# Optimization experiments

Hardware: AMD Instinct MI355X
Metric: run time of the kernel (lower is better)

Reference implementation:

```python
import jax, jax.numpy as jnp
import numpy as np

N = 100000
CTX = 128
TGT = 32
H = 64
FUS = H + H // 2  # 96
E1 = 1600000
E2 = 800000
LN_EPS = 1e-5


def _gelu(x):
    return jax.nn.gelu(x, approximate=False)  # torch default is exact erf GELU


def _layer_norm(x, g, b):
    mu = jnp.mean(x, -1, keepdims=True)
    xc = x - mu
    var = jnp.mean(xc * xc, -1, keepdims=True)
    return xc * jax.lax.rsqrt(var + LN_EPS) * g + b


def _gcn_conv(x, W, b, ei, n):
    # PyG GCNConv: x' = D^-1/2 (A + I) D^-1/2 (x W) + b, with unit edge weights.
    h = x @ W  # [N, out]
    src, dst = ei[0], ei[1]
    deg = jnp.zeros((n,), h.dtype).at[dst].add(1.0) + 1.0  # +1 for self-loop
    dinv = jax.lax.rsqrt(deg)
    norm = dinv[src] * dinv[dst]  # [E]
    agg = jnp.zeros_like(h).at[dst].add(h[src] * norm[:, None])
    agg = agg + h * (dinv * dinv)[:, None]  # self-loop messages
    return agg + b


def setup_inputs() -> dict:
    key = jax.random.key(0)
    ks = jax.random.split(key, 32)
    def lin(k, fan_in, fan_out):
        s = 1.0 / np.sqrt(fan_in)
        k1, k2 = jax.random.split(k)
        return (jax.random.uniform(k1, (fan_in, fan_out), jnp.float32, -s, s),
                jax.random.uniform(k2, (fan_out,), jnp.float32, -s, s))
    inp = {}
    inp['context'] = jax.random.normal(ks[0], (N, CTX), jnp.float32)
    inp['target'] = jax.random.normal(ks[1], (N, TGT), jnp.float32)
    inp['mask'] = jax.random.bernoulli(ks[2], 0.5, (N, TGT))
    inp['adj_ei'] = jax.random.randint(ks[3], (2, E1), 0, N, jnp.int64 if jax.config.jax_enable_x64 else jnp.int32)
    inp['transit_ei'] = jax.random.randint(ks[4], (2, E2), 0, N, jnp.int64 if jax.config.jax_enable_x64 else jnp.int32)
    inp['mask_token'] = jax.random.normal(ks[5], (1, TGT), jnp.float32) * 0.01
    inp['ce_W1'], inp['ce_b1'] = lin(ks[6], CTX, H)
    inp['ce_g'] = jnp.ones((H,), jnp.float32)
    inp['ce_beta'] = jnp.zeros((H,), jnp.float32)
    inp['ce_W2'], inp['ce_b2'] = lin(ks[7], H, H)
    inp['te_W'], inp['te_b'] = lin(ks[8], TGT, H // 2)
    inp['g1_W'], inp['g1_b'] = lin(ks[9], FUS, H)
    inp['g2_W'], inp['g2_b'] = lin(ks[10], H, H)
    inp['t1_W'], inp['t1_b'] = lin(ks[11], FUS, H)
    inp['t2_W'], inp['t2_b'] = lin(ks[12], H, H)
    inp['alpha'] = jnp.float32(0.5)
    inp['h_W1'], inp['h_b1'] = lin(ks[13], H + FUS, H)
    inp['h_g'] = jnp.ones((H,), jnp.float32)
    inp['h_beta'] = jnp.zeros((H,), jnp.float32)
    inp['h_W2'], inp['h_b2'] = lin(ks[14], H, TGT)
    return inp


def reference(context, target, mask, adj_ei, transit_ei, mask_token,
              ce_W1, ce_b1, ce_g, ce_beta, ce_W2, ce_b2,
              te_W, te_b,
              g1_W, g1_b, g2_W, g2_b,
              t1_W, t1_b, t2_W, t2_b,
              alpha,
              h_W1, h_b1, h_g, h_beta, h_W2, h_b2):
    n = context.shape[0]
    # context encoder (eval mode: dropout is identity)
    c = _gelu(_layer_norm(context @ ce_W1 + ce_b1, ce_g, ce_beta))
    ctx = _gelu(c @ ce_W2 + ce_b2)
    # masked target encoder
    m = mask.astype(target.dtype)
    masked_t = target * (1.0 - m) + mask_token * m
    tgt = _gelu(masked_t @ te_W + te_b)
    fused = jnp.concatenate([ctx, tgt], -1)  # [N, 96]
    # spatial branch
    h1 = _gelu(_gcn_conv(fused, g1_W, g1_b, adj_ei, n))
    h_sp = _gcn_conv(h1, g2_W, g2_b, adj_ei, n)
    # transit branch
    h2 = _gelu(_gcn_conv(fused, t1_W, t1_b, transit_ei, n))
    h_tr = _gcn_conv(h2, t2_W, t2_b, transit_ei, n)
    a = jax.nn.sigmoid(alpha)
    h = a * h_sp + (1.0 - a) * h_tr
    z = jnp.concatenate([h, fused], -1)  # [N, 160]
    z = _gelu(_layer_norm(z @ h_W1 + h_b1, h_g, h_beta))
    return z @ h_W2 + h_b2  # [N, 32]
```

## Files before the change

kernel.cpp:

```cpp
#include <hip/hip_runtime.h>
#include <math.h>


#define LN_EPS 1e-5f
#define NRANGES 512
#define RMASK 511
#define LSHIFT 9
#define PASSP_EDGES 8192
#define GSTRIDE 16

typedef __attribute__((ext_vector_type(8))) short short8;
typedef __attribute__((ext_vector_type(4))) float float4v;
typedef __attribute__((ext_vector_type(4))) unsigned short ushort4v;

__device__ __forceinline__ float gelu_exact(float x) {
    return 0.5f * x * (1.0f + erff(x * 0.70710678118654752440f));
}

__device__ __forceinline__ float qsum16(float v) {
#pragma unroll
    for (int m = 1; m < 16; m <<= 1)
        v += __shfl_xor(v, m, 64);
    return v;
}

__device__ __forceinline__ int load_edge(const void* ei, int is32, long idx) {
    return is32 ? ((const int*)ei)[idx] : (int)((const long long*)ei)[idx];
}

__device__ __forceinline__ unsigned short f32_to_bf16(float f) {
    unsigned int x = __float_as_uint(f);
    x += 0x7fffu + ((x >> 16) & 1u);
    return (unsigned short)(x >> 16);
}
__device__ __forceinline__ float bf16_to_f32(unsigned short u) {
    return __uint_as_float((unsigned int)u << 16);
}

__device__ __forceinline__ void load_dst4(const void* ei1, int e1, const void* ei2, int e2,
                                          int n, int is32, int base, int nv, int nd[4]) {
    if (is32 && nv == 4) {
        if (base + 3 < e1 && (((e1 + base) & 3) == 0)) {
            int4 v = *(const int4*)((const int*)ei1 + (size_t)e1 + base);
            nd[0] = v.x; nd[1] = v.y; nd[2] = v.z; nd[3] = v.w;
            return;
        }
        if (base >= e1 && (((e2 + base - e1) & 3) == 0)) {
            int4 v = *(const int4*)((const int*)ei2 + (size_t)e2 + (base - e1));
            nd[0] = v.x + n; nd[1] = v.y + n; nd[2] = v.z + n; nd[3] = v.w + n;
            return;
        }
    }
#pragma unroll
    for (int u = 0; u < 4; ++u) {
        int i = base + u;
        if (u >= nv) { nd[u] = -1; continue; }
        if (i < e1) nd[u] = load_edge(ei1, is32, (long)e1 + i);
        else        nd[u] = load_edge(ei2, is32, (long)e2 + (i - e1)) + n;
    }
}

__device__ __forceinline__ void load_src4(const void* ei1, int e1, const void* ei2, int e2,
                                          int is32, int base, int nv, int ns[4]) {
    if (is32 && nv == 4) {
        if (base + 3 < e1 && ((base & 3) == 0)) {
            int4 v = *(const int4*)((const int*)ei1 + base);
            ns[0] = v.x; ns[1] = v.y; ns[2] = v.z; ns[3] = v.w;
            return;
        }
        if (base >= e1 && (((base - e1) & 3) == 0)) {
            int4 v = *(const int4*)((const int*)ei2 + (base - e1));
            ns[0] = v.x; ns[1] = v.y; ns[2] = v.z; ns[3] = v.w;
            return;
        }
    }
#pragma unroll
    for (int u = 0; u < 4; ++u) {
        int i = base + u;
        if (u >= nv) { ns[u] = 0; continue; }
        if (i < e1) ns[u] = load_edge(ei1, is32, i);
        else        ns[u] = load_edge(ei2, is32, (long)(i - e1));
    }
}

__global__ __launch_bounds__(256) void detect_kernel(const unsigned char* __restrict__ mask_bytes,
                                                     const int* __restrict__ ei_words,
                                                     int* __restrict__ flags,
                                                     int* __restrict__ gcur, int cap) {
    if (blockIdx.x == 0) {
        __shared__ int f0, f1;
        if (threadIdx.x == 0) { f0 = 0; f1 = 0; }
        __syncthreads();
        int i = threadIdx.x;
        if ((i & 3) != 0 && mask_bytes[i] != 0) f0 = 1;
        if (i < 64 && ei_words[2 * i + 1] != 0) f1 = 1;
        __syncthreads();
        if (threadIdx.x == 0) { flags[0] = f0; flags[1] = f1; }
    } else {
        int r = (blockIdx.x - 1) * 256 + threadIdx.x;
        if (r < NRANGES) gcur[r * GSTRIDE] = r * cap;
    }
}

__device__ __forceinline__ void passp_body(
    const void* ei1, int e1, const void* ei2, int e2,
    int n, const int* flags, int* gcur, int cap, unsigned* ebuf, int sbits, int bid)
{
    __shared__ int hist[NRANGES];
    __shared__ int base[NRANGES];
    const int E = e1 + e2;
    const int is32 = flags[1];
    const int b0 = bid * PASSP_EDGES;
    const int bend = (b0 + PASSP_EDGES < E) ? b0 + PASSP_EDGES : E;

    for (int k = threadIdx.x; k < NRANGES; k += 256) hist[k] = 0;
    __syncthreads();

    int nd[32], rk[32];
#pragma unroll
    for (int j = 0; j < 8; ++j) {
        int bi = b0 + j * 1024 + (int)threadIdx.x * 4;
        int nv = bend - bi; nv = (nv < 0) ? 0 : (nv > 4 ? 4 : nv);
        load_dst4(ei1, e1, ei2, e2, n, is32, bi, nv, &nd[j * 4]);
#pragma unroll
        for (int u = 0; u < 4; ++u)
            if (u < nv) rk[j * 4 + u] = atomicAdd(&hist[nd[j * 4 + u] & RMASK], 1);
    }
    __syncthreads();

    for (int r = threadIdx.x; r < NRANGES; r += 256) {
        int c = hist[r];
        base[r] = c ? atomicAdd(&gcur[r * GSTRIDE], c) : 0;
    }
    __syncthreads();

#pragma unroll
    for (int j = 0; j < 8; ++j) {
        int bi = b0 + j * 1024 + (int)threadIdx.x * 4;
        int nv = bend - bi; nv = (nv < 0) ? 0 : (nv > 4 ? 4 : nv);
        int sv[4];
        load_src4(ei1, e1, ei2, e2, is32, bi, nv, sv);
#pragma unroll
        for (int u = 0; u < 4; ++u) {
            if (u < nv) {
                int d = nd[j * 4 + u];
                int r = d & RMASK;
                int pos = base[r] + rk[j * 4 + u];
                if (pos < (r + 1) * cap)
                    ebuf[pos] = (unsigned)sv[u] | ((unsigned)(d >> LSHIFT) << sbits);
            }
        }
    }
}

__device__ __forceinline__ void prep_body(
    const float* context, const float* target, const void* mask, const int* flags,
    const float* mask_token, const float* te_W, const float* te_b,
    unsigned short* ctxb, unsigned short* fused, int n, int bid)
{
    __shared__ float tbuf[32][32];
    int w = threadIdx.x >> 6;
    int j = threadIdx.x & 63;
    int r0 = __builtin_amdgcn_readfirstlane(bid * 32 + w * 8);
    if (r0 >= n) return;

    const float4* src = (const float4*)(context + (size_t)r0 * 128);
    ushort4v* dst = (ushort4v*)(ctxb + (size_t)r0 * 128);
#pragma unroll
    for (int p = 0; p < 4; ++p) {
        float4 v = src[p * 64 + j];
        ushort4v o;
        o.x = f32_to_bf16(v.x); o.y = f32_to_bf16(v.y);
        o.z = f32_to_bf16(v.z); o.w = f32_to_bf16(v.w);
        dst[p * 64 + j] = o;
    }

    int tr = j >> 5;
    int tj = j & 31;
#pragma unroll
    for (int rr = 0; rr < 4; ++rr) {
        int r = tr + rr * 2;
        long mi = (long)(r0 + r) * 32 + tj;
        int mraw = flags[0] ? (int)((const unsigned char*)mask)[mi]
                            : ((const int*)mask)[mi];
        float m = mraw ? 1.0f : 0.0f;
        tbuf[w * 8 + r][tj] = target[mi] * (1.0f - m) + mask_token[tj] * m;
    }

#pragma unroll
    for (int rr = 0; rr < 4; ++rr) {
        int r = tr + rr * 2;
        float y3 = te_b[tj];
#pragma unroll
        for (int k = 0; k < 32; ++k)
            y3 = fmaf(tbuf[w * 8 + r][k], te_W[k * 32 + tj], y3);
        fused[(long)(r0 + r) * 96 + 64 + tj] = f32_to_bf16(gelu_exact(y3));
    }
}

__global__ __launch_bounds__(256) void passp_prep_kernel(
    const void* __restrict__ ei1, int e1, const void* __restrict__ ei2, int e2,
    int n, const int* __restrict__ flags, int* __restrict__ gcur, int cap,
    unsigned* __restrict__ ebuf, int sbits, int ppBlocks,
    const float* __restrict__ context, const float* __restrict__ target,
    const void* __restrict__ mask, const float* __restrict__ mask_token,
    const float* __restrict__ te_W, const float* __restrict__ te_b,
    unsigned short* __restrict__ ctxb, unsigned short* __restrict__ fused)
{
    if ((int)blockIdx.x < ppBlocks)
        passp_body(ei1, e1, ei2, e2, n, flags, gcur, cap, ebuf, sbits, blockIdx.x);
    else
        prep_body(context, target, mask, flags, mask_token, te_W, te_b,
                  ctxb, fused, n, blockIdx.x - ppBlocks);
}

__device__ __forceinline__ void rscan_body(const int* gcur, int cap,
                                           int* rstart, int* rowptr, int n2) {
    __shared__ int ws[256];
    int t = threadIdx.x;
    int i0 = 2 * t, i1 = 2 * t + 1;
    int a0 = gcur[i0 * GSTRIDE] - i0 * cap;
    int a1 = gcur[i1 * GSTRIDE] - i1 * cap;
    ws[t] = a0 + a1;
    __syncthreads();
    for (int off = 1; off < 256; off <<= 1) {
        int v = (t >= off) ? ws[t - off] : 0;
        __syncthreads();
        if (t >= off) ws[t] += v;
        __syncthreads();
    }
    int ex = t ? ws[t - 1] : 0;
    rstart[i0] = ex;
    rstart[i1] = ex + a0;
    if (t == 255) { rstart[NRANGES] = ws[255]; rowptr[n2] = ws[255]; }
}

__device__ __forceinline__ void mfma_ln_body(
    const unsigned short* x, const float* W, const float* bias, const float* g,
    const float* beta, unsigned short* y, int n, int bid, int nblk)
{
    constexpr int K = 128, KS = K / 32, STRIDE = K + 8;
    __shared__ __align__(16) unsigned short wt[64 * STRIDE];
    int n0 = threadIdx.x & 63;
    int kk = threadIdx.x >> 6;
    for (int k = kk; k < K; k += 4)
        wt[n0 * STRIDE + k] = f32_to_bf16(W[k * 64 + n0]);
    __syncthreads();

    int w = threadIdx.x >> 6;
    int lane = threadIdx.x & 63;
    int c = lane & 15;
    int q = lane >> 4;

    short8 bfrag[KS][4];
#pragma unroll
    for (int s = 0; s < KS; ++s)
#pragma unroll
        for (int nt = 0; nt < 4; ++nt)
            bfrag[s][nt] = *(const short8*)&wt[(nt * 16 + c) * STRIDE + s * 32 + q * 8];

    float bs[4], gs[4], be[4];
#pragma unroll
    for (int nt = 0; nt < 4; ++nt) {
        bs[nt] = bias[nt * 16 + c];
        gs[nt] = g[nt * 16 + c];
        be[nt] = beta[nt * 16 + c];
    }

    int T = n >> 4;
    int stride = nblk * 4;
    for (int t = __builtin_amdgcn_readfirstlane(bid * 4 + w); t < T; t += stride) {
        int r0 = t << 4;
        const unsigned short* xa = x + (size_t)(r0 + c) * K + q * 8;
        float4v acc[4] = {{0,0,0,0},{0,0,0,0},{0,0,0,0},{0,0,0,0}};
#pragma unroll
        for (int s = 0; s < KS; ++s) {
            short8 a = *(const short8*)(xa + s * 32);
#pragma unroll
            for (int nt = 0; nt < 4; ++nt)
                acc[nt] = __builtin_amdgcn_mfma_f32_16x16x32_bf16(a, bfrag[s][nt], acc[nt], 0, 0, 0);
        }
#pragma unroll
        for (int reg = 0; reg < 4; ++reg) {
            float v0 = acc[0][reg] + bs[0];
            float v1 = acc[1][reg] + bs[1];
            float v2 = acc[2][reg] + bs[2];
            float v3 = acc[3][reg] + bs[3];
            float mean = qsum16((v0 + v1) + (v2 + v3)) * (1.0f / 64.0f);
            float x0 = v0 - mean, x1 = v1 - mean, x2 = v2 - mean, x3 = v3 - mean;
            float var = qsum16((x0 * x0 + x1 * x1) + (x2 * x2 + x3 * x3)) * (1.0f / 64.0f);
            float rstd = rsqrtf(var + LN_EPS);
            size_t row = (size_t)(r0 + q * 4 + reg) * 64;
            y[row + 0 * 16 + c] = f32_to_bf16(gelu_exact(x0 * rstd * gs[0] + be[0]));
            y[row + 1 * 16 + c] = f32_to_bf16(gelu_exact(x1 * rstd * gs[1] + be[1]));
            y[row + 2 * 16 + c] = f32_to_bf16(gelu_exact(x2 * rstd * gs[2] + be[2]));
            y[row + 3 * 16 + c] = f32_to_bf16(gelu_exact(x3 * rstd * gs[3] + be[3]));
        }
    }
}

__global__ __launch_bounds__(256) void ln_rscan_kernel(
    const unsigned short* __restrict__ x, const float* __restrict__ W,
    const float* __restrict__ bias, const float* __restrict__ g,
    const float* __restrict__ beta, unsigned short* __restrict__ y, int n, int nblk,
    const int* __restrict__ gcur, int cap, int* __restrict__ rstart,
    int* __restrict__ rowptr, int n2)
{
    if ((int)blockIdx.x == nblk)
        rscan_body(gcur, cap, rstart, rowptr, n2);
    else
        mfma_ln_body(x, W, bias, g, beta, y, n, blockIdx.x, nblk);
}

__device__ __forceinline__ void passq_body(
    const int* rstart, const unsigned* ebuf, int cap, int n2, int sbits,
    int* rowptr, int* rowcnt, float* dinv, int* srcs, int g)
{
    __shared__ int deg[NRANGES];
    __shared__ int cur[NRANGES];
    __shared__ int ws[256];
    const int t = threadIdx.x;
    const int gbase = rstart[g];
    const int total = rstart[g + 1] - gbase;
    const unsigned* eb = ebuf + (size_t)g * cap;
    const unsigned smask = (1u << sbits) - 1u;

    deg[2 * t] = 0; deg[2 * t + 1] = 0;
    __syncthreads();
    for (int i = t; i < total; i += 256)
        atomicAdd(&deg[eb[i] >> sbits], 1);
    __syncthreads();

    int a0 = deg[2 * t], a1 = deg[2 * t + 1];
    ws[t] = a0 + a1;
    __syncthreads();
    for (int off = 1; off < 256; off <<= 1) {
        int v = (t >= off) ? ws[t - off] : 0;
        __syncthreads();
        if (t >= off) ws[t] += v;
        __syncthreads();
    }
    int ex = t ? ws[t - 1] : 0;
    cur[2 * t] = ex;
    cur[2 * t + 1] = ex + a0;
    int node0 = ((2 * t) << LSHIFT) | g;
    int node1 = ((2 * t + 1) << LSHIFT) | g;
    if (node0 < n2) { rowptr[node0] = gbase + ex;      rowcnt[node0] = a0; dinv[node0] = rsqrtf((float)a0 + 1.0f); }
    if (node1 < n2) { rowptr[node1] = gbase + ex + a0; rowcnt[node1] = a1; dinv[node1] = rsqrtf((float)a1 + 1.0f); }
    __syncthreads();

    for (int i = t; i < total; i += 256) {
        unsigned e = eb[i];
        int rk = atomicAdd(&cur[e >> sbits], 1);
        srcs[gbase + rk] = (int)(e & smask);
    }
}

__device__ __forceinline__ void mfma_gelu_body(
    const unsigned short* x, const float* W, const float* bias,
    unsigned short* y, int n, int bid, int nblk)
{
    constexpr int K = 64, KS = K / 32, STRIDE = K + 8;
    __shared__ __align__(16) unsigned short wt[64 * STRIDE];
    int n0 = threadIdx.x & 63;
    int kk = threadIdx.x >> 6;
    for (int k = kk; k < K; k += 4)
        wt[n0 * STRIDE + k] = f32_to_bf16(W[k * 64 + n0]);
    __syncthreads();

    int w = threadIdx.x >> 6;
    int lane = threadIdx.x & 63;
    int c = lane & 15;
    int q = lane >> 4;

    short8 bfrag[KS][4];
#pragma unroll
    for (int s = 0; s < KS; ++s)
#pragma unroll
        for (int nt = 0; nt < 4; ++nt)
            bfrag[s][nt] = *(const short8*)&wt[(nt * 16 + c) * STRIDE + s * 32 + q * 8];

    float bs[4];
#pragma unroll
    for (int nt = 0; nt < 4; ++nt) bs[nt] = bias[nt * 16 + c];

    int T = n >> 4;
    int stride = nblk * 4;
    for (int t = __builtin_amdgcn_readfirstlane(bid * 4 + w); t < T; t += stride) {
        int r0 = t << 4;
        const unsigned short* xa = x + (size_t)(r0 + c) * K + q * 8;
        float4v acc[4] = {{0,0,0,0},{0,0,0,0},{0,0,0,0},{0,0,0,0}};
#pragma unroll
        for (int s = 0; s < KS; ++s) {
            short8 a = *(const short8*)(xa + s * 32);
#pragma unroll
            for (int nt = 0; nt < 4; ++nt)
                acc[nt] = __builtin_amdgcn_mfma_f32_16x16x32_bf16(a, bfrag[s][nt], acc[nt], 0, 0, 0);
        }
#pragma unroll
        for (int nt = 0; nt < 4; ++nt)
#pragma unroll
            for (int reg = 0; reg < 4; ++reg)
                y[(size_t)(r0 + q * 4 + reg) * 96 + nt * 16 + c] =
                    f32_to_bf16(gelu_exact(acc[nt][reg] + bs[nt]));
    }
}

__global__ __launch_bounds__(256) void passq_gelu_kernel(
    const int* __restrict__ rstart, const unsigned* __restrict__ ebuf, int cap, int n2,
    int sbits, int* __restrict__ rowptr, int* __restrict__ rowcnt,
    float* __restrict__ dinv, int* __restrict__ srcs,
    const unsigned short* __restrict__ x, const float* __restrict__ W,
    const float* __restrict__ bias, unsigned short* __restrict__ y, int n, int nblk)
{
    if ((int)blockIdx.x < NRANGES)
        passq_body(rstart, ebuf, cap, n2, sbits, rowptr, rowcnt, dinv, srcs, blockIdx.x);
    else
        mfma_gelu_body(x, W, bias, y, n, blockIdx.x - NRANGES, nblk);
}

__global__ __launch_bounds__(256) void mm_l1_dual_kernel(
    const unsigned short* __restrict__ x, const float* __restrict__ Wg,
    const float* __restrict__ Wt, const float* __restrict__ dinv,
    unsigned short* __restrict__ yg, unsigned short* __restrict__ yt, int n)
{
    constexpr int K = 96, KS = K / 32, STRIDE = K + 8;
    __shared__ __align__(16) unsigned short wtg[64 * STRIDE];
    __shared__ __align__(16) unsigned short wtt[64 * STRIDE];
    int n0 = threadIdx.x & 63;
    int kk = threadIdx.x >> 6;
    for (int k = kk; k < K; k += 4) {
        wtg[n0 * STRIDE + k] = f32_to_bf16(Wg[k * 64 + n0]);
        wtt[n0 * STRIDE + k] = f32_to_bf16(Wt[k * 64 + n0]);
    }
    __syncthreads();

    int w = threadIdx.x >> 6;
    int lane = threadIdx.x & 63;
    int c = lane & 15;
    int q = lane >> 4;

    short8 bg[KS][4], bt[KS][4];
#pragma unroll
    for (int s = 0; s < KS; ++s)
#pragma unroll
        for (int nt = 0; nt < 4; ++nt) {
            bg[s][nt] = *(const short8*)&wtg[(nt * 16 + c) * STRIDE + s * 32 + q * 8];
            bt[s][nt] = *(const short8*)&wtt[(nt * 16 + c) * STRIDE + s * 32 + q * 8];
        }

    int T = n >> 4;
    int stride = gridDim.x * 4;
    for (int t = __builtin_amdgcn_readfirstlane(blockIdx.x * 4 + w); t < T; t += stride) {
        int r0 = t << 4;
        const unsigned short* xa = x + (size_t)(r0 + c) * K + q * 8;
        float4v ag[4] = {{0,0,0,0},{0,0,0,0},{0,0,0,0},{0,0,0,0}};
        float4v at[4] = {{0,0,0,0},{0,0,0,0},{0,0,0,0},{0,0,0,0}};
#pragma unroll
        for (int s = 0; s < KS; ++s) {
            short8 a = *(const short8*)(xa + s * 32);
#pragma unroll
            for (int nt = 0; nt < 4; ++nt) {
                ag[nt] = __builtin_amdgcn_mfma_f32_16x16x32_bf16(a, bg[s][nt], ag[nt], 0, 0, 0);
                at[nt] = __builtin_amdgcn_mfma_f32_16x16x32_bf16(a, bt[s][nt], at[nt], 0, 0, 0);
            }
        }
        float sg[4], st[4];
#pragma unroll
        for (int reg = 0; reg < 4; ++reg) {
            sg[reg] = dinv[r0 + q * 4 + reg];
            st[reg] = dinv[n + r0 + q * 4 + reg];
        }
#pragma unroll
        for (int nt = 0; nt < 4; ++nt)
#pragma unroll
            for (int reg = 0; reg < 4; ++reg) {
                size_t row = (size_t)(r0 + q * 4 + reg) * 64 + nt * 16 + c;
                yg[row] = f32_to_bf16(ag[nt][reg] * sg[reg]);
                yt[row] = f32_to_bf16(at[nt][reg] * st[reg]);
            }
    }
}

__device__ __forceinline__ void mm64_body(const unsigned short* x, const float* W,
                                          const float* scale, unsigned short* y,
                                          int n, int bid, int nblk) {
    constexpr int K = 64, KS = K / 32, STRIDE = K + 8;
    __shared__ __align__(16) unsigned short wt[64 * STRIDE];
    int n0 = threadIdx.x & 63;
    int kk = threadIdx.x >> 6;
    for (int k = kk; k < K; k += 4)
        wt[n0 * STRIDE + k] = f32_to_bf16(W[k * 64 + n0]);
    __syncthreads();

    int w = threadIdx.x >> 6;
    int lane = threadIdx.x & 63;
    int c = lane & 15;
    int q = lane >> 4;

    short8 bfrag[KS][4];
#pragma unroll
    for (int s = 0; s < KS; ++s)
#pragma unroll
        for (int nt = 0; nt < 4; ++nt)
            bfrag[s][nt] = *(const short8*)&wt[(nt * 16 + c) * STRIDE + s * 32 + q * 8];

    int T = n >> 4;
    int stride = nblk * 4;
    for (int t = __builtin_amdgcn_readfirstlane(bid * 4 + w); t < T; t += stride) {
        int r0 = t << 4;
        const unsigned short* xa = x + (size_t)(r0 + c) * K + q * 8;
        float4v acc[4] = {{0,0,0,0},{0,0,0,0},{0,0,0,0},{0,0,0,0}};
#pragma unroll
        for (int s = 0; s < KS; ++s) {
            short8 a = *(const short8*)(xa + s * 32);
#pragma unroll
            for (int nt = 0; nt < 4; ++nt)
                acc[nt] = __builtin_amdgcn_mfma_f32_16x16x32_bf16(a, bfrag[s][nt], acc[nt], 0, 0, 0);
        }
        float sc[4];
#pragma unroll
        for (int reg = 0; reg < 4; ++reg)
            sc[reg] = scale[r0 + q * 4 + reg];
#pragma unroll
        for (int nt = 0; nt < 4; ++nt)
#pragma unroll
            for (int reg = 0; reg < 4; ++reg)
                y[(size_t)(r0 + q * 4 + reg) * 64 + nt * 16 + c] = f32_to_bf16(acc[nt][reg] * sc[reg]);
    }
}

__global__ __launch_bounds__(256) void mm_l2_kernel(
    const unsigned short* __restrict__ xg, const unsigned short* __restrict__ xt,
    const float* __restrict__ Wg, const float* __restrict__ Wt,
    const float* __restrict__ dinv,
    unsigned short* __restrict__ yg, unsigned short* __restrict__ yt, int n, int nblk)
{
    if ((int)blockIdx.x < nblk)
        mm64_body(xg, Wg, dinv, yg, n, blockIdx.x, nblk);
    else
        mm64_body(xt, Wt, dinv + n, yt, n, blockIdx.x - nblk, nblk);
}

__device__ __forceinline__ float gather_row(const int* srcs, const unsigned short* lin,
                                            int beg, int cnt, int j) {
    float acc = 0.0f;
    for (int base = beg; base < beg + cnt; base += 64) {
        int c2 = beg + cnt - base;
        if (c2 > 64) c2 = 64;
        int sj = (j < c2) ? srcs[base + j] : 0;
        int t = 0;
        for (; t + 8 <= c2; t += 8) {
            float v[8];
#pragma unroll
            for (int u = 0; u < 8; ++u) {
                int s = __shfl(sj, t + u, 64);
                v[u] = bf16_to_f32(lin[(long)s * 64 + j]);
            }
            acc += ((v[0] + v[1]) + (v[2] + v[3])) + ((v[4] + v[5]) + (v[6] + v[7]));
        }
        for (; t < c2; ++t) {
            int s = __shfl(sj, t, 64);
            acc += bf16_to_f32(lin[(long)s * 64 + j]);
        }
    }
    return acc;
}

__global__ __launch_bounds__(256) void gather_l1_kernel(
    const int* __restrict__ rowptr, const int* __restrict__ rowcnt,
    const int* __restrict__ srcs, const float* __restrict__ dinv,
    const unsigned short* __restrict__ ling, const unsigned short* __restrict__ lint,
    const float* __restrict__ bg, const float* __restrict__ bt,
    unsigned short* __restrict__ h1g, unsigned short* __restrict__ h1t, int n)
{
    int w = threadIdx.x >> 6;
    int j = threadIdx.x & 63;
    int node = __builtin_amdgcn_readfirstlane(blockIdx.x * 4 + w);
    if (node >= n) return;
    long oi = (long)node * 64 + j;

    float ag = gather_row(srcs, ling, rowptr[node], rowcnt[node], j);
    float pg = fmaf(dinv[node], ag + bf16_to_f32(ling[oi]), bg[j]);
    h1g[oi] = f32_to_bf16(gelu_exact(pg));

    int tn = n + node;
    float at = gather_row(srcs, lint, rowptr[tn], rowcnt[tn], j);
    float pt = fmaf(dinv[tn], at + bf16_to_f32(lint[oi]), bt[j]);
    h1t[oi] = f32_to_bf16(gelu_exact(pt));
}

__global__ __launch_bounds__(256) void gather_l2_kernel(
    const int* __restrict__ rowptr, const int* __restrict__ rowcnt,
    const int* __restrict__ srcs, const float* __restrict__ dinv,
    const unsigned short* __restrict__ ling, const unsigned short* __restrict__ lint,
    const float* __restrict__ bg, const float* __restrict__ bt,
    const float* __restrict__ alpha_ptr, unsigned short* __restrict__ hb, int n)
{
    int w = threadIdx.x >> 6;
    int j = threadIdx.x & 63;
    int node = __builtin_amdgcn_readfirstlane(blockIdx.x * 4 + w);
    if (node >= n) return;
    long oi = (long)node * 64 + j;

    float ag = gather_row(srcs, ling, rowptr[node], rowcnt[node], j);
    float pg = fmaf(dinv[node], ag + bf16_to_f32(ling[oi]), bg[j]);

    int tn = n + node;
    float at = gather_row(srcs, lint, rowptr[tn], rowcnt[tn], j);
    float pt = fmaf(dinv[tn], at + bf16_to_f32(lint[oi]), bt[j]);

    float a = 1.0f / (1.0f + expf(-alpha_ptr[0]));
    hb[oi] = f32_to_bf16(a * pg + (1.0f - a) * pt);
}

__global__ __launch_bounds__(256) void head_mfma_kernel(
    const unsigned short* __restrict__ hb, const unsigned short* __restrict__ fused,
    const float* __restrict__ h_W1, const float* __restrict__ h_b1,
    const float* __restrict__ h_g, const float* __restrict__ h_beta,
    const float* __restrict__ h_W2, const float* __restrict__ h_b2,
    float* __restrict__ out, int n)
{
    constexpr int ST1 = 168;
    constexpr int ST2 = 72;
    __shared__ __align__(16) unsigned short wt1[64 * ST1];
    __shared__ __align__(16) unsigned short wt2[32 * ST2];
    __shared__ __align__(16) unsigned short zl[4][16 * ST2];

    int n0 = threadIdx.x & 63;
    int kk = threadIdx.x >> 6;
    for (int k = kk; k < 160; k += 4)
        wt1[n0 * ST1 + k] = f32_to_bf16(h_W1[k * 64 + n0]);
    if (n0 < 32)
        for (int k = kk; k < 64; k += 4)
            wt2[n0 * ST2 + k] = f32_to_bf16(h_W2[k * 32 + n0]);
    __syncthreads();

    int w = threadIdx.x >> 6;
    int lane = threadIdx.x & 63;
    int c = lane & 15;
    int q = lane >> 4;

    short8 b1f[5][4];
#pragma unroll
    for (int s = 0; s < 5; ++s)
#pragma unroll
        for (int nt = 0; nt < 4; ++nt)
            b1f[s][nt] = *(const short8*)&wt1[(nt * 16 + c) * ST1 + s * 32 + q * 8];
    short8 b2f[2][2];
#pragma unroll
    for (int s = 0; s < 2; ++s)
#pragma unroll
        for (int nt = 0; nt < 2; ++nt)
            b2f[s][nt] = *(const short8*)&wt2[(nt * 16 + c) * ST2 + s * 32 + q * 8];

    float bs[4], gs[4], be[4];
#pragma unroll
    for (int nt = 0; nt < 4; ++nt) {
        bs[nt] = h_b1[nt * 16 + c];
        gs[nt] = h_g[nt * 16 + c];
        be[nt] = h_beta[nt * 16 + c];
    }
    float b2s[2];
#pragma unroll
    for (int nt = 0; nt < 2; ++nt) b2s[nt] = h_b2[nt * 16 + c];

    unsigned short* zw = zl[w];
    int T = n >> 4;
    int stride = gridDim.x * 4;
    for (int t = __builtin_amdgcn_readfirstlane(blockIdx.x * 4 + w); t < T; t += stride) {
        int r0 = t << 4;
        const unsigned short* xh = hb + (size_t)(r0 + c) * 64 + q * 8;
        const unsigned short* xf = fused + (size_t)(r0 + c) * 96 + q * 8;
        float4v acc[4] = {{0,0,0,0},{0,0,0,0},{0,0,0,0},{0,0,0,0}};
#pragma unroll
        for (int s = 0; s < 2; ++s) {
            short8 a = *(const short8*)(xh + s * 32);
#pragma unroll
            for (int nt = 0; nt < 4; ++nt)
                acc[nt] = __builtin_amdgcn_mfma_f32_16x16x32_bf16(a, b1f[s][nt], acc[nt], 0, 0, 0);
        }
#pragma unroll
        for (int s = 0; s < 3; ++s) {
            short8 a = *(const short8*)(xf + s * 32);
#pragma unroll
            for (int nt = 0; nt < 4; ++nt)
                acc[nt] = __builtin_amdgcn_mfma_f32_16x16x32_bf16(a, b1f[2 + s][nt], acc[nt], 0, 0, 0);
        }
#pragma unroll
        for (int reg = 0; reg < 4; ++reg) {
            float v0 = acc[0][reg] + bs[0];
            float v1 = acc[1][reg] + bs[1];
            float v2 = acc[2][reg] + bs[2];
            float v3 = acc[3][reg] + bs[3];
            float mean = qsum16((v0 + v1) + (v2 + v3)) * (1.0f / 64.0f);
            float x0 = v0 - mean, x1 = v1 - mean, x2 = v2 - mean, x3 = v3 - mean;
            float var = qsum16((x0 * x0 + x1 * x1) + (x2 * x2 + x3 * x3)) * (1.0f / 64.0f);
            float rstd = rsqrtf(var + LN_EPS);
            int row = q * 4 + reg;
            zw[row * ST2 + 0 * 16 + c] = f32_to_bf16(gelu_exact(x0 * rstd * gs[0] + be[0]));
            zw[row * ST2 + 1 * 16 + c] = f32_to_bf16(gelu_exact(x1 * rstd * gs[1] + be[1]));
            zw[row * ST2 + 2 * 16 + c] = f32_to_bf16(gelu_exact(x2 * rstd * gs[2] + be[2]));
            zw[row * ST2 + 3 * 16 + c] = f32_to_bf16(gelu_exact(x3 * rstd * gs[3] + be[3]));
        }
        float4v acc2[2] = {{0,0,0,0},{0,0,0,0}};
#pragma unroll
        for (int s = 0; s < 2; ++s) {
            short8 a2 = *(const short8*)&zw[c * ST2 + s * 32 + q * 8];
#pragma unroll
            for (int nt = 0; nt < 2; ++nt)
                acc2[nt] = __builtin_amdgcn_mfma_f32_16x16x32_bf16(a2, b2f[s][nt], acc2[nt], 0, 0, 0);
        }
#pragma unroll
        for (int nt = 0; nt < 2; ++nt)
#pragma unroll
            for (int reg = 0; reg < 4; ++reg)
                out[(size_t)(r0 + q * 4 + reg) * 32 + nt * 16 + c] = acc2[nt][reg] + b2s[nt];
    }
}

extern "C" void kernel_launch(void* const* d_in, const int* in_sizes, int n_in,
                              void* d_out, int out_size, void* d_ws, size_t ws_size,
                              hipStream_t stream) {
    const float* context    = (const float*)d_in[0];
    const float* target     = (const float*)d_in[1];
    const void*  mask       = d_in[2];
    const void*  adj_ei     = d_in[3];
    const void*  tr_ei      = d_in[4];
    const float* mask_token = (const float*)d_in[5];
    const float* ce_W1 = (const float*)d_in[6];
    const float* ce_b1 = (const float*)d_in[7];
    const float* ce_g  = (const float*)d_in[8];
    const float* ce_be = (const float*)d_in[9];
    const float* ce_W2 = (const float*)d_in[10];
    const float* ce_b2 = (const float*)d_in[11];
    const float* te_W  = (const float*)d_in[12];
    const float* te_b  = (const float*)d_in[13];
    const float* g1_W  = (const float*)d_in[14];
    const float* g1_b  = (const float*)d_in[15];
    const float* g2_W  = (const float*)d_in[16];
    const float* g2_b  = (const float*)d_in[17];
    const float* t1_W  = (const float*)d_in[18];
    const float* t1_b  = (const float*)d_in[19];
    const float* t2_W  = (const float*)d_in[20];
    const float* t2_b  = (const float*)d_in[21];
    const float* alpha = (const float*)d_in[22];
    const float* h_W1  = (const float*)d_in[23];
    const float* h_b1  = (const float*)d_in[24];
    const float* h_g   = (const float*)d_in[25];
    const float* h_be  = (const float*)d_in[26];
    const float* h_W2  = (const float*)d_in[27];
    const float* h_b2  = (const float*)d_in[28];

    const int N  = in_sizes[0] / 128;
    const int E1 = in_sizes[3] / 2;
    const int E2 = in_sizes[4] / 2;
    const int E  = E1 + E2;
    const int N2 = 2 * N;

    int sbits = 1;
    while ((1 << sbits) < N) ++sbits;

    long expct = (E + NRANGES - 1) / NRANGES;
    int cap = (int)((expct * 4 / 3) & ~255L);
    long avail = (long)N * 128;
    int capmax = (int)((avail / ((long)NRANGES * 4)) & ~255L);
    if (cap > capmax) cap = capmax;
    if (cap < 1024) cap = 1024;

    char* p = (char*)d_ws;
    int*   flags  = (int*)p;                    p += 256;
    unsigned short* ctxb  = (unsigned short*)p; p += (size_t)N * 128 * 2;
    unsigned short* fused = (unsigned short*)p; p += (size_t)N * 96 * 2;
    unsigned short* cb    = (unsigned short*)p; p += (size_t)N * 64 * 2;
    unsigned short* lin   = (unsigned short*)p; p += (size_t)N * 64 * 2;
    unsigned short* h1    = (unsigned short*)p; p += (size_t)N * 64 * 2;
    unsigned short* hb    = (unsigned short*)p; p += (size_t)N * 64 * 2;
    float* hacc   = (float*)p;                  p += (size_t)N * 64 * 4;
    float* dinv   = (float*)p;                  p += (size_t)N2 * 4;
    int*   rowptr = (int*)p;                    p += (size_t)(N2 + 64) * 4;
    int*   rowcnt = (int*)p;                    p += (size_t)(N2 + 64) * 4;
    int*   gcur   = (int*)p;                    p += (size_t)NRANGES * GSTRIDE * 4;
    int*   rstart = (int*)p;                    p += (size_t)(NRANGES + 8) * 4;
    int*   srcs   = (int*)p;                    p += (size_t)E * 4;
    unsigned*       ebuf = (unsigned*)hacc;
    unsigned short* h1t  = (unsigned short*)((char*)hacc + (size_t)N * 128);
    unsigned short* h1g  = h1;
    unsigned short* ling = lin;
    unsigned short* lint = cb;
    float* out    = (float*)d_out;

    const unsigned rowBlocks32 = (unsigned)((N + 31) / 32);
    const unsigned nodeBlocks  = (unsigned)((N + 3) / 4);
    const unsigned ppBlocks    = (unsigned)((E + PASSP_EDGES - 1) / PASSP_EDGES);
    const unsigned mmBlocks    = 391;

    detect_kernel<<<3, 256, 0, stream>>>((const unsigned char*)mask, (const int*)adj_ei,
                                         flags, gcur, cap);
    passp_prep_kernel<<<ppBlocks + rowBlocks32, 256, 0, stream>>>(
        adj_ei, E1, tr_ei, E2, N, flags, gcur, cap, ebuf, sbits, (int)ppBlocks,
        context, target, mask, mask_token, te_W, te_b, ctxb, fused);
    ln_rscan_kernel<<<mmBlocks + 1, 256, 0, stream>>>(
        ctxb, ce_W1, ce_b1, ce_g, ce_be, cb, N, (int)mmBlocks,
        gcur, cap, rstart, rowptr, N2);
    passq_gelu_kernel<<<NRANGES + mmBlocks, 256, 0, stream>>>(
        rstart, ebuf, cap, N2, sbits, rowptr, rowcnt, dinv, srcs,
        cb, ce_W2, ce_b2, fused, N, (int)mmBlocks);

    mm_l1_dual_kernel<<<mmBlocks, 256, 0, stream>>>(fused, g1_W, t1_W, dinv, ling, lint, N);
    gather_l1_kernel<<<nodeBlocks, 256, 0, stream>>>(rowptr, rowcnt, srcs, dinv,
                                                     ling, lint, g1_b, t1_b, h1g, h1t, N);
    mm_l2_kernel<<<2 * mmBlocks, 256, 0, stream>>>(h1g, h1t, g2_W, t2_W, dinv,
                                                   ling, lint, N, (int)mmBlocks);
    gather_l2_kernel<<<nodeBlocks, 256, 0, stream>>>(rowptr, rowcnt, srcs, dinv,
                                                     ling, lint, g2_b, t2_b, alpha, hb, N);

    head_mfma_kernel<<<mmBlocks, 256, 0, stream>>>(hb, fused, h_W1, h_b1, h_g, h_be,
                                                   h_W2, h_b2, out, N);
}
```

Before: 484.6 us.

## Gather four nodes per wavefront with 16 lanes and 8-byte vector loads

The CSR gather kernels now give each node a 16-lane quarter-wave instead of a full 64-lane wave. Each lane loads four bf16 features as one uint2 and keeps four accumulators, with edge indices broadcast by 16-wide shuffles. The aim is to cut load instruction count and the idle lanes that low-degree nodes leave, and to raise memory-level parallelism across nodes. In exchange, nodes in the same wave have different degrees, so their loop trip counts diverge, and accumulation order changes slightly.

```diff
diff --git a/kernel.cpp b/kernel.cpp
--- a/kernel.cpp
+++ b/kernel.cpp
@@ -36,6 +36,8 @@
 __device__ __forceinline__ float bf16_to_f32(unsigned short u) {
     return __uint_as_float((unsigned int)u << 16);
 }
+__device__ __forceinline__ float bflo(unsigned x) { return __uint_as_float(x << 16); }
+__device__ __forceinline__ float bfhi(unsigned x) { return __uint_as_float(x & 0xffff0000u); }
 
 __device__ __forceinline__ void load_dst4(const void* ei1, int e1, const void* ei2, int e2,
                                           int n, int is32, int base, int nv, int nd[4]) {
@@ -542,29 +544,34 @@
         mm64_body(xt, Wt, dinv + n, yt, n, blockIdx.x - nblk, nblk);
 }
 
-__device__ __forceinline__ float gather_row(const int* srcs, const unsigned short* lin,
-                                            int beg, int cnt, int j) {
-    float acc = 0.0f;
-    for (int base = beg; base < beg + cnt; base += 64) {
-        int c2 = beg + cnt - base;
-        if (c2 > 64) c2 = 64;
-        int sj = (j < c2) ? srcs[base + j] : 0;
+__device__ __forceinline__ void gather4(const int* __restrict__ srcs,
+                                        const unsigned short* __restrict__ lin,
+                                        int beg, int cnt, int l, float acc[4]) {
+    for (int base = 0; base < cnt; base += 16) {
+        int c2 = cnt - base;
+        if (c2 > 16) c2 = 16;
+        int sj = (l < c2) ? srcs[beg + base + l] : 0;
         int t = 0;
-        for (; t + 8 <= c2; t += 8) {
-            float v[8];
-#pragma unroll
-            for (int u = 0; u < 8; ++u) {
-                int s = __shfl(sj, t + u, 64);
-                v[u] = bf16_to_f32(lin[(long)s * 64 + j]);
+        for (; t + 4 <= c2; t += 4) {
+            uint2 v[4];
+#pragma unroll
+            for (int u = 0; u < 4; ++u) {
+                int s = __shfl(sj, t + u, 16);
+                v[u] = *(const uint2*)(lin + (size_t)((unsigned)s * 64u + (unsigned)(l * 4)));
             }
-            acc += ((v[0] + v[1]) + (v[2] + v[3])) + ((v[4] + v[5]) + (v[6] + v[7]));
+#pragma unroll
+            for (int u = 0; u < 4; ++u) {
+                acc[0] += bflo(v[u].x); acc[1] += bfhi(v[u].x);
+                acc[2] += bflo(v[u].y); acc[3] += bfhi(v[u].y);
+            }
         }
         for (; t < c2; ++t) {
-            int s = __shfl(sj, t, 64);
-            acc += bf16_to_f32(lin[(long)s * 64 + j]);
-        }
-    }
-    return acc;
+            int s = __shfl(sj, t, 16);
+            uint2 vv = *(const uint2*)(lin + (size_t)((unsigned)s * 64u + (unsigned)(l * 4)));
+            acc[0] += bflo(vv.x); acc[1] += bfhi(vv.x);
+            acc[2] += bflo(vv.y); acc[3] += bfhi(vv.y);
+        }
+    }
 }
 
 __global__ __launch_bounds__(256) void gather_l1_kernel(
@@ -575,19 +582,45 @@
     unsigned short* __restrict__ h1g, unsigned short* __restrict__ h1t, int n)
 {
     int w = threadIdx.x >> 6;
-    int j = threadIdx.x & 63;
-    int node = __builtin_amdgcn_readfirstlane(blockIdx.x * 4 + w);
+    int lane = threadIdx.x & 63;
+    int g = lane >> 4;
+    int l = lane & 15;
+    int node = blockIdx.x * 16 + w * 4 + g;
     if (node >= n) return;
-    long oi = (long)node * 64 + j;
-
-    float ag = gather_row(srcs, ling, rowptr[node], rowcnt[node], j);
-    float pg = fmaf(dinv[node], ag + bf16_to_f32(ling[oi]), bg[j]);
-    h1g[oi] = f32_to_bf16(gelu_exact(pg));
-
-    int tn = n + node;
-    float at = gather_row(srcs, lint, rowptr[tn], rowcnt[tn], j);
-    float pt = fmaf(dinv[tn], at + bf16_to_f32(lint[oi]), bt[j]);
-    h1t[oi] = f32_to_bf16(gelu_exact(pt));
+
+    float4 b4g = ((const float4*)bg)[l];
+    float4 b4t = ((const float4*)bt)[l];
+    unsigned off = (unsigned)node * 64u + (unsigned)(l * 4);
+
+    {
+        float acc[4] = {0, 0, 0, 0};
+        gather4(srcs, ling, rowptr[node], rowcnt[node], l, acc);
+        uint2 sv = *(const uint2*)(ling + off);
+        acc[0] += bflo(sv.x); acc[1] += bfhi(sv.x);
+        acc[2] += bflo(sv.y); acc[3] += bfhi(sv.y);
+        float dd = dinv[node];
+        ushort4v o;
+        o.x = f32_to_bf16(gelu_exact(fmaf(dd, acc[0], b4g.x)));
+        o.y = f32_to_bf16(gelu_exact(fmaf(dd, acc[1], b4g.y)));
+        o.z = f32_to_bf16(gelu_exact(fmaf(dd, acc[2], b4g.z)));
+        o.w = f32_to_bf16(gelu_exact(fmaf(dd, acc[3], b4g.w)));
+        *(ushort4v*)(h1g + off) = o;
+    }
+    {
+        int tn = n + node;
+        float acc[4] = {0, 0, 0, 0};
+        gather4(srcs, lint, rowptr[tn], rowcnt[tn], l, acc);
+        uint2 sv = *(const uint2*)(lint + off);
+        acc[0] += bflo(sv.x); acc[1] += bfhi(sv.x);
+        acc[2] += bflo(sv.y); acc[3] += bfhi(sv.y);
+        float dd = dinv[tn];
+        ushort4v o;
+        o.x = f32_to_bf16(gelu_exact(fmaf(dd, acc[0], b4t.x)));
+        o.y = f32_to_bf16(gelu_exact(fmaf(dd, acc[1], b4t.y)));
+        o.z = f32_to_bf16(gelu_exact(fmaf(dd, acc[2], b4t.z)));
+        o.w = f32_to_bf16(gelu_exact(fmaf(dd, acc[3], b4t.w)));
+        *(ushort4v*)(h1t + off) = o;
+    }
 }
 
 __global__ __launch_bounds__(256) void gather_l2_kernel(
@@ -598,20 +631,46 @@
     const float* __restrict__ alpha_ptr, unsigned short* __restrict__ hb, int n)
 {
     int w = threadIdx.x >> 6;
-    int j = threadIdx.x & 63;
-    int node = __builtin_amdgcn_readfirstlane(blockIdx.x * 4 + w);
+    int lane = threadIdx.x & 63;
+    int g = lane >> 4;
+    int l = lane & 15;
+    int node = blockIdx.x * 16 + w * 4 + g;
     if (node >= n) return;
-    long oi = (long)node * 64 + j;
-
-    float ag = gather_row(srcs, ling, rowptr[node], rowcnt[node], j);
-    float pg = fmaf(dinv[node], ag + bf16_to_f32(ling[oi]), bg[j]);
-
-    int tn = n + node;
-    float at = gather_row(srcs, lint, rowptr[tn], rowcnt[tn], j);
-    float pt = fmaf(dinv[tn], at + bf16_to_f32(lint[oi]), bt[j]);
-
+
+    float4 b4g = ((const float4*)bg)[l];
+    float4 b4t = ((const float4*)bt)[l];
+    unsigned off = (unsigned)node * 64u + (unsigned)(l * 4);
+
+    float pg[4], pt[4];
+    {
+        float acc[4] = {0, 0, 0, 0};
+        gather4(srcs, ling, rowptr[node], rowcnt[node], l, acc);
+        uint2 sv = *(const uint2*)(ling + off);
+        acc[0] += bflo(sv.x); acc[1] += bfhi(sv.x);
+        acc[2] += bflo(sv.y); acc[3] += bfhi(sv.y);
+        float dd = dinv[node];
+        pg[0] = fmaf(dd, acc[0], b4g.x); pg[1] = fmaf(dd, acc[1], b4g.y);
+        pg[2] = fmaf(dd, acc[2], b4g.z); pg[3] = fmaf(dd, acc[3], b4g.w);
+    }
+    {
+        int tn = n + node;
+        float acc[4] = {0, 0, 0, 0};
+        gather4(srcs, lint, rowptr[tn], rowcnt[tn], l, acc);
+        uint2 sv = *(const uint2*)(lint + off);
+        acc[0] += bflo(sv.x); acc[1] += bfhi(sv.x);
+        acc[2] += bflo(sv.y); acc[3] += bfhi(sv.y);
+        float dd = dinv[tn];
+        pt[0] = fmaf(dd, acc[0], b4t.x); pt[1] = fmaf(dd, acc[1], b4t.y);
+        pt[2] = fmaf(dd, acc[2], b4t.z); pt[3] = fmaf(dd, acc[3], b4t.w);
+    }
     float a = 1.0f / (1.0f + expf(-alpha_ptr[0]));
-    hb[oi] = f32_to_bf16(a * pg + (1.0f - a) * pt);
+    float b = 1.0f - a;
+    ushort4v o;
+    o.x = f32_to_bf16(a * pg[0] + b * pt[0]);
+    o.y = f32_to_bf16(a * pg[1] + b * pt[1]);
+    o.z = f32_to_bf16(a * pg[2] + b * pt[2]);
+    o.w = f32_to_bf16(a * pg[3] + b * pt[3]);
+    *(ushort4v*)(hb + off) = o;
 }
 
 __global__ __launch_bounds__(256) void head_mfma_kernel(
@@ -791,7 +850,7 @@
     float* out    = (float*)d_out;
 
     const unsigned rowBlocks32 = (unsigned)((N + 31) / 32);
-    const unsigned nodeBlocks  = (unsigned)((N + 3) / 4);
+    const unsigned nodeBlocks16 = (unsigned)((N + 15) / 16);
     const unsigned ppBlocks    = (unsigned)((E + PASSP_EDGES - 1) / PASSP_EDGES);
     const unsigned mmBlocks    = 391;
 
@@ -808,12 +867,12 @@
         cb, ce_W2, ce_b2, fused, N, (int)mmBlocks);
 
     mm_l1_dual_kernel<<<mmBlocks, 256, 0, stream>>>(fused, g1_W, t1_W, dinv, ling, lint, N);
-    gather_l1_kernel<<<nodeBlocks, 256, 0, stream>>>(rowptr, rowcnt, srcs, dinv,
-                                                     ling, lint, g1_b, t1_b, h1g, h1t, N);
+    gather_l1_kernel<<<nodeBlocks16, 256, 0, stream>>>(rowptr, rowcnt, srcs, dinv,
+                                                       ling, lint, g1_b, t1_b, h1g, h1t, N);
     mm_l2_kernel<<<2 * mmBlocks, 256, 0, stream>>>(h1g, h1t, g2_W, t2_W, dinv,
                                                    ling, lint, N, (int)mmBlocks);
-    gather_l2_kernel<<<nodeBlocks, 256, 0, stream>>>(rowptr, rowcnt, srcs, dinv,
-                                                     ling, lint, g2_b, t2_b, alpha, hb, N);
+    gather_l2_kernel<<<nodeBlocks16, 256, 0, stream>>>(rowptr, rowcnt, srcs, dinv,
+                                                       ling, lint, g2_b, t2_b, alpha, hb, N);
 
     head_mfma_kernel<<<mmBlocks, 256, 0, stream>>>(hb, fused, h_W1, h_b1, h_g, h_be,
                                                    h_W2, h_b2, out, N);
```

Result: faster. 420.0 us (-13.3%).
